# Performance work log

Hardware: AMD Instinct MI355X
Metric: run time of the kernel (lower is better)

Reference implementation:

```python
import jax, jax.numpy as jnp
import numpy as np

N_SIGMA = 1
K_MAX = 8          # max number of non-zero instance ids
FG_W = 1.0         # foreground_weight
W_INST, W_VAR, W_SEED = 1.0, 10.0, 1.0


def _lovasz_hinge_flat(logits, labels_f):
    # logits, labels_f: [P] flat; standard Lovasz hinge (descending-error sort)
    signs = 2.0 * labels_f - 1.0
    errors = 1.0 - logits * signs
    perm = jnp.argsort(-errors)
    errors_sorted = errors[perm]
    gt_sorted = labels_f[perm]
    gts = gt_sorted.sum()
    cum = jnp.cumsum(gt_sorted)
    intersection = gts - cum
    union = gts + jnp.cumsum(1.0 - gt_sorted)
    jaccard = 1.0 - intersection / union
    grad = jnp.concatenate([jaccard[:1], jaccard[1:] - jaccard[:-1]])
    return jnp.sum(jax.nn.relu(errors_sorted) * jax.lax.stop_gradient(grad))


def _spatial_emb_loss(prediction, instances, labels):
    B, C, H, W = prediction.shape
    inst = instances[:, 0]  # [B,H,W]
    # coordinate buffer: linspace over the full 1024x2048 grid, then sliced
    xm = jnp.linspace(0.0, 2.0, 2048)[:W]
    ym = jnp.linspace(0.0, 1.0, 1024)[:H]
    xym = jnp.stack([jnp.broadcast_to(xm[None, :], (H, W)),
                     jnp.broadcast_to(ym[:, None], (H, W))])  # [2,H,W]
    ids = jnp.arange(1, K_MAX + 1)

    def per_image(pred, ins, lab):
        spatial_emb = jnp.tanh(pred[0:2]) + xym            # [2,H,W]
        sigma = pred[2]                                     # [H,W] (n_sigma=1)
        seed = jax.nn.sigmoid(pred[3])                      # [H,W]
        bg = (lab == 0)
        seed_loss_bg = jnp.sum(jnp.where(bg, seed ** 2, 0.0))
        masks = (ins[None] == ids[:, None, None])           # [K,H,W]
        mf = masks.astype(pred.dtype)
        counts = mf.sum((1, 2))                             # [K]
        present = counts > 0
        cnt = jnp.maximum(counts, 1.0)
        # to_center=True: center = mean of xym over instance pixels
        center = jnp.einsum('chw,khw->kc', xym, mf) / cnt[:, None]   # [K,2]
        s_mean = jnp.einsum('hw,khw->k', sigma, mf) / cnt            # [K]
        var_k = jnp.einsum('khw,khw->k',
                           (sigma[None] - jax.lax.stop_gradient(s_mean)[:, None, None]) ** 2,
                           mf) / cnt
        s_exp = jnp.exp(10.0 * s_mean)                                # [K]
        d2 = jnp.sum((spatial_emb[None] - center[:, :, None, None]) ** 2, axis=1)  # [K,H,W]
        dist = jnp.exp(-s_exp[:, None, None] * d2)                    # [K,H,W]
        lov = jax.vmap(_lovasz_hinge_flat)(2.0 * dist.reshape(K_MAX, -1) - 1.0,
                                           mf.reshape(K_MAX, -1))     # [K]
        seed_fg = jnp.einsum('khw,khw->k',
                             (seed[None] - jax.lax.stop_gradient(dist)) ** 2, mf)
        objf = jnp.maximum(present.sum().astype(pred.dtype), 1.0)
        inst_loss = jnp.where(present, lov, 0.0).sum() / objf
        var_loss = jnp.where(present, var_k, 0.0).sum() / objf
        seed_loss = (seed_loss_bg + FG_W * jnp.where(present, seed_fg, 0.0).sum()) / (H * W)
        return W_INST * inst_loss + W_VAR * var_loss + W_SEED * seed_loss

    per = jax.vmap(per_image)(prediction, inst, labels)
    return per.mean() + 0.0 * prediction.sum()


def setup_inputs() -> dict:
    key = jax.random.key(0)
    k1, k2, k3 = jax.random.split(key, 3)
    B, H, W = 4, 512, 1024
    prediction = jax.random.normal(k1, (B, 2 + N_SIGMA + 1, H, W), dtype=jnp.float32)
    instances = jax.random.randint(k2, (B, 1, H, W), 0, K_MAX + 1, dtype=jnp.int32)
    labels = jax.random.randint(k3, (B, H, W), 0, 2, dtype=jnp.int32)
    return {"prediction": prediction, "instances": instances, "labels": labels}


def reference(prediction, instances, labels):
    return _spatial_emb_loss(prediction, instances, labels)
```

## Files before the change

kernel.cpp:

```cpp
#include <hip/hip_runtime.h>
#include <math.h>

namespace {
constexpr int B_ = 4, K_ = 8, W_ = 1024;
constexpr int N_ = 512 * 1024;
constexpr int M_ = 128;
constexpr int MP_ = M_ + 1;
constexpr int BK_ = B_ * K_;
constexpr int KM_ = K_ * M_;

constexpr int HB_ = 512;
constexpr int HBPB_ = HB_ / B_;
constexpr int HCH_ = N_ / HBPB_;
constexpr int SB_ = 1024;
constexpr int SBPB_ = SB_ / B_;
constexpr int SCH_ = N_ / SBPB_;
constexpr int NSTAT = 41;
constexpr int NHC_ = 4;

constexpr size_t PART_BYTES = (size_t)HB_ * KM_ * 4;
constexpr size_t SFG_OFF_B  = PART_BYTES;
constexpr size_t PSTAT_OFF_B = SFG_OFF_B + (size_t)BK_ * HBPB_ * 4;
constexpr size_t WSF_OFF_B  = PSTAT_OFF_B + (size_t)B_ * NSTAT * SBPB_ * 4;

constexpr int CNT_OFF  = 0;
constexpr int OBJF_OFF = 32;
}

__device__ __forceinline__ float fsigmoid_(float x) { return 1.0f / (1.0f + __expf(-x)); }
__device__ __forceinline__ float ftanh_(float x) { return 1.0f - 2.0f / (__expf(2.0f * x) + 1.0f); }

__global__ __launch_bounds__(256) void stats_kernel(const float* __restrict__ pred,
                                                    const int* __restrict__ inst,
                                                    const int* __restrict__ lab,
                                                    float* __restrict__ pstat,
                                                    float* __restrict__ out) {
    int tid = threadIdx.x;
    if (blockIdx.x == 0 && tid == 0) out[0] = 0.0f;
    int b = blockIdx.x >> 8;
    int blk = blockIdx.x & (SBPB_ - 1);
    int pix0 = blk * SCH_;

    const float* sigp = pred + ((long long)b * 4 + 2) * N_;
    const float* p3p  = pred + ((long long)b * 4 + 3) * N_;
    const int*   insp = inst + (long long)b * N_;
    const int*   labp = lab  + (long long)b * N_;

    float acc[NSTAT];
#pragma unroll
    for (int i = 0; i < NSTAT; i++) acc[i] = 0.0f;

#pragma unroll
    for (int it = 0; it < SCH_ / (256 * 4); it++) {
        int base = pix0 + (it * 256 + tid) * 4;
        float4 sg = *(const float4*)(sigp + base);
        float4 q3 = *(const float4*)(p3p + base);
        int4 in4 = *(const int4*)(insp + base);
        int4 lb4 = *(const int4*)(labp + base);
        float ss[4] = {sg.x, sg.y, sg.z, sg.w};
        float qq[4] = {q3.x, q3.y, q3.z, q3.w};
        int ii[4] = {in4.x, in4.y, in4.z, in4.w};
        int ll[4] = {lb4.x, lb4.y, lb4.z, lb4.w};
#pragma unroll
        for (int j = 0; j < 4; j++) {
            int pix = base + j;
            float xm = (float)(pix & (W_ - 1)) * (2.0f / 2047.0f);
            float ym = (float)(pix >> 10) * (1.0f / 1023.0f);
            float seed = fsigmoid_(qq[j]);
            if (ll[j] == 0) acc[40] += seed * seed;
            float s = ss[j];
#pragma unroll
            for (int k = 0; k < K_; k++) {
                float m = (ii[j] == k + 1) ? 1.0f : 0.0f;
                acc[k * 5]     += m;
                acc[k * 5 + 1] += m * xm;
                acc[k * 5 + 2] += m * ym;
                acc[k * 5 + 3] += m * s;
                acc[k * 5 + 4] += m * s * s;
            }
        }
    }
#pragma unroll
    for (int i = 0; i < NSTAT; i++) {
        float v = acc[i];
#pragma unroll
        for (int off = 32; off; off >>= 1) v += __shfl_down(v, off, 64);
        acc[i] = v;
    }
    __shared__ float xw[4][NSTAT];
    if ((tid & 63) == 0) {
        int w = tid >> 6;
#pragma unroll
        for (int i = 0; i < NSTAT; i++) xw[w][i] = acc[i];
    }
    __syncthreads();
    if (tid < NSTAT)
        pstat[((b * NSTAT + tid) << 8) + blk] =
            xw[0][tid] + xw[1][tid] + xw[2][tid] + xw[3][tid];
}

__global__ __launch_bounds__(256) void hist_kernel(const float* __restrict__ pred,
                                                   const int* __restrict__ inst,
                                                   const float* __restrict__ pstat,
                                                   float* __restrict__ wsf,
                                                   unsigned int* __restrict__ partial,
                                                   float* __restrict__ sfgpart,
                                                   float* __restrict__ out) {
    __shared__ float sq[NSTAT][4];
    __shared__ float ssum[NSTAT];
    __shared__ float prm[K_][4];
    __shared__ float svar[K_];
    __shared__ int spres[K_];
    __shared__ unsigned int hsh[NHC_][K_ * MP_];
    __shared__ float xfg[4][K_];

    int tid = threadIdx.x;
    int b = blockIdx.x >> 7;
    int blk = blockIdx.x & (HBPB_ - 1);
    int pix0 = blk * HCH_;

    if (tid < NSTAT * 4) {
        int row = tid >> 2, q = tid & 3;
        const float4* p = (const float4*)(pstat + ((size_t)(b * NSTAT + row) << 8)) + q * 16;
        float4 a = {0, 0, 0, 0};
#pragma unroll
        for (int j = 0; j < 16; j++) {
            float4 v = p[j];
            a.x += v.x; a.y += v.y; a.z += v.z; a.w += v.w;
        }
        sq[row][q] = (a.x + a.y) + (a.z + a.w);
    }
    for (int i = tid; i < NHC_ * K_ * MP_; i += 256) (&hsh[0][0])[i] = 0u;
    __syncthreads();
    if (tid < NSTAT) ssum[tid] = (sq[tid][0] + sq[tid][1]) + (sq[tid][2] + sq[tid][3]);
    __syncthreads();
    if (tid < K_) {
        float counts = ssum[tid * 5];
        float cnt = fmaxf(counts, 1.0f);
        float smean = ssum[tid * 5 + 3] / cnt;
        prm[tid][0] = ssum[tid * 5 + 1] / cnt;
        prm[tid][1] = ssum[tid * 5 + 2] / cnt;
        prm[tid][2] = expf(10.0f * smean);
        prm[tid][3] = counts;
        if (blk == 0) {
            svar[tid] = (counts > 0.0f) ? ssum[tid * 5 + 4] / cnt - smean * smean : 0.0f;
            spres[tid] = counts > 0.0f ? 1 : 0;
            wsf[CNT_OFF + b * K_ + tid] = counts;
        }
    }
    __syncthreads();
    if (blk == 0 && tid == 0) {
        float np = 0.0f, vl = 0.0f;
#pragma unroll
        for (int k = 0; k < K_; k++) { np += (float)spres[k]; vl += svar[k]; }
        float objf = fmaxf(np, 1.0f);
        wsf[OBJF_OFF + b] = objf;
        atomicAdd(out, (10.0f * vl / objf + ssum[40] / (float)N_) * (1.0f / (float)B_));
    }

    float cx[K_], cy[K_], sxp[K_];
    bool prs[K_];
#pragma unroll
    for (int k = 0; k < K_; k++) {
        cx[k] = prm[k][0]; cy[k] = prm[k][1]; sxp[k] = prm[k][2];
        prs[k] = prm[k][3] > 0.0f;
    }
    unsigned int* hpriv = &hsh[tid & 3][0];

    const float* p0p = pred + ((long long)b * 4) * N_;
    const float* p1p = p0p + N_;
    const float* p3p = p0p + 3LL * N_;
    const int* insp = inst + (long long)b * N_;

    float sfg[K_];
#pragma unroll
    for (int k = 0; k < K_; k++) sfg[k] = 0.0f;

#pragma unroll
    for (int it = 0; it < HCH_ / (256 * 4); it++) {
        int base = pix0 + (it * 256 + tid) * 4;
        float4 a0 = *(const float4*)(p0p + base);
        float4 a1 = *(const float4*)(p1p + base);
        float4 a3 = *(const float4*)(p3p + base);
        int4 in4 = *(const int4*)(insp + base);
        float v0[4] = {a0.x, a0.y, a0.z, a0.w};
        float v1[4] = {a1.x, a1.y, a1.z, a1.w};
        float v3[4] = {a3.x, a3.y, a3.z, a3.w};
        int ii[4] = {in4.x, in4.y, in4.z, in4.w};
#pragma unroll
        for (int j = 0; j < 4; j++) {
            int pix = base + j;
            float sex = ftanh_(v0[j]) + (float)(pix & (W_ - 1)) * (2.0f / 2047.0f);
            float sey = ftanh_(v1[j]) + (float)(pix >> 10) * (1.0f / 1023.0f);
            float seed = fsigmoid_(v3[j]);
            int ins = ii[j];
#pragma unroll
            for (int k = 0; k < K_; k++) {
                if (prs[k]) {
                    float dx = sex - cx[k];
                    float dy = sey - cy[k];
                    float dist = __expf(-sxp[k] * (dx * dx + dy * dy));
                    bool fg = (ins == k + 1);
                    int ib = (int)fminf(128.0f * dist, 127.0f);
                    int bin = fg ? 127 - ib : ib;
                    atomicAdd(hpriv + (k * MP_ + bin), fg ? 0x10001u : 1u);
                    if (fg) { float d = seed - dist; sfg[k] += d * d; }
                }
            }
        }
    }
    __syncthreads();

    unsigned int* gp = partial + (size_t)blockIdx.x * KM_;
    for (int i = tid; i < KM_; i += 256) {
        int r = (i >> 7) * MP_ + (i & (M_ - 1));
        gp[i] = hsh[0][r] + hsh[1][r] + hsh[2][r] + hsh[3][r];
    }

#pragma unroll
    for (int k = 0; k < K_; k++) {
        float v = sfg[k];
#pragma unroll
        for (int off = 32; off; off >>= 1) v += __shfl_down(v, off, 64);
        sfg[k] = v;
    }
    if ((tid & 63) == 0) {
        int w = tid >> 6;
#pragma unroll
        for (int k = 0; k < K_; k++) xfg[w][k] = sfg[k];
    }
    __syncthreads();
    if (tid < K_)
        sfgpart[(size_t)(b * K_ + tid) * HBPB_ + blk] =
            xfg[0][tid] + xfg[1][tid] + xfg[2][tid] + xfg[3][tid];
}

__global__ __launch_bounds__(1024) void lovasz_kernel(const unsigned int* __restrict__ partial,
                                                      const float* __restrict__ sfgpart,
                                                      const float* __restrict__ wsf,
                                                      float* __restrict__ out) {
    int bk = blockIdx.x;
    int b = bk >> 3, k = bk & 7;
    int tid = threadIdx.x;
    int bin = tid & (M_ - 1), grp = tid >> 7;
    constexpr int PER = HBPB_ / 8;

    const unsigned int* p = partial +
        (size_t)(b * HBPB_ + grp * PER) * KM_ + k * M_ + bin;
    unsigned int n = 0, f = 0;
#pragma unroll
    for (int j = 0; j < PER; j++) {
        unsigned int v = p[(size_t)j * KM_];
        n += v & 0xffffu;
        f += v >> 16;
    }

    __shared__ unsigned int gn[8][M_], gf[8][M_];
    __shared__ float lovp;
    __shared__ float xs[2];
    gn[grp][bin] = n; gf[grp][bin] = f;
    __syncthreads();

    float pcnt = wsf[CNT_OFF + bk];
    float pp = fmaxf(pcnt, 1.0f);

    if (tid < 64) {
        unsigned long long p0 = 0ull, p1 = 0ull;
#pragma unroll
        for (int g = 0; g < 8; g++) {
            uint2 vn = *(const uint2*)&gn[g][2 * tid];
            uint2 vf = *(const uint2*)&gf[g][2 * tid];
            p0 += ((unsigned long long)vn.x << 32) | (unsigned long long)vf.x;
            p1 += ((unsigned long long)vn.y << 32) | (unsigned long long)vf.y;
        }
        unsigned long long T = p0 + p1;
#pragma unroll
        for (int off = 1; off < 64; off <<= 1) {
            unsigned long long t = __shfl_down(T, off, 64);
            if (tid + off < 64) T += t;
        }
        unsigned long long S0 = T;
        unsigned long long S1 = T - p0;
        float acc;
        {
            unsigned int R = (unsigned int)(S0 >> 32), F = (unsigned int)S0;
            float J = (R == 0) ? 0.0f : (1.0f - (pp - (float)F) / (pp + (float)(R - F)));
            acc = (tid == 0 ? 0.5f : 1.0f) * J;
        }
        {
            unsigned int R = (unsigned int)(S1 >> 32), F = (unsigned int)S1;
            float J = (R == 0) ? 0.0f : (1.0f - (pp - (float)F) / (pp + (float)(R - F)));
            acc += J;
        }
#pragma unroll
        for (int off = 32; off; off >>= 1) acc += __shfl_down(acc, off, 64);
        if (tid == 0) lovp = acc;
    } else if (tid >= 256 && tid < 384) {
        float sv = sfgpart[(size_t)bk * HBPB_ + (tid - 256)];
#pragma unroll
        for (int off = 32; off; off >>= 1) sv += __shfl_down(sv, off, 64);
        if ((tid & 63) == 0) xs[(tid - 256) >> 6] = sv;
    }
    __syncthreads();

    if (tid == 0 && pcnt > 0.0f) {
        float lov = lovp * (2.0f / (float)M_);
        float sfgt = xs[0] + xs[1];
        float objf = wsf[OBJF_OFF + b];
        atomicAdd(out, (lov / objf + sfgt / (float)N_) * (1.0f / (float)B_));
    }
}

extern "C" void kernel_launch(void* const* d_in, const int* in_sizes, int n_in,
                              void* d_out, int out_size, void* d_ws, size_t ws_size,
                              hipStream_t stream) {
    const float* pred = (const float*)d_in[0];
    const int* inst = (const int*)d_in[1];
    const int* lab = (const int*)d_in[2];
    float* out = (float*)d_out;

    unsigned int* partial = (unsigned int*)d_ws;
    float* sfgpart = (float*)((char*)d_ws + SFG_OFF_B);
    float* pstat = (float*)((char*)d_ws + PSTAT_OFF_B);
    float* wsf = (float*)((char*)d_ws + WSF_OFF_B);

    stats_kernel<<<SB_, 256, 0, stream>>>(pred, inst, lab, pstat, out);
    hist_kernel<<<HB_, 256, 0, stream>>>(pred, inst, pstat, wsf, partial, sfgpart, out);
    lovasz_kernel<<<BK_, 1024, 0, stream>>>(partial, sfgpart, wsf, out);
}
```

Measured before the change: 116.5 us.

## Fuse Lovasz finalization into hist kernel via last-blocks ticket counter

Removes the separate lovasz_kernel launch. Each hist block takes a per-image atomic ticket, and the last four blocks of each image spin-wait until all blocks of that image have finished. Each of those blocks then reduces the partial histograms and sfg sums for two instance ids and computes the Lovasz term. This saves one launch and its gap, but the final reduction now runs in only 16 blocks of 256 threads instead of 32 blocks of 1024 threads. It also relies on spin-waiting, which needs all blocks of an image to be resident or to finish without deadlock.

```diff
diff --git a/kernel.cpp b/kernel.cpp
--- a/kernel.cpp
+++ b/kernel.cpp
@@ -17,14 +17,12 @@
 constexpr int SCH_ = N_ / SBPB_;
 constexpr int NSTAT = 41;
 constexpr int NHC_ = 4;
+constexpr int NFIN_ = 4;
 
 constexpr size_t PART_BYTES = (size_t)HB_ * KM_ * 4;
 constexpr size_t SFG_OFF_B  = PART_BYTES;
 constexpr size_t PSTAT_OFF_B = SFG_OFF_B + (size_t)BK_ * HBPB_ * 4;
-constexpr size_t WSF_OFF_B  = PSTAT_OFF_B + (size_t)B_ * NSTAT * SBPB_ * 4;
-
-constexpr int CNT_OFF  = 0;
-constexpr int OBJF_OFF = 32;
+constexpr size_t CTR_OFF_B  = PSTAT_OFF_B + (size_t)B_ * NSTAT * SBPB_ * 4;
 }
 
 __device__ __forceinline__ float fsigmoid_(float x) { return 1.0f / (1.0f + __expf(-x)); }
@@ -34,9 +32,13 @@
                                                     const int* __restrict__ inst,
                                                     const int* __restrict__ lab,
                                                     float* __restrict__ pstat,
+                                                    unsigned int* __restrict__ ctr,
                                                     float* __restrict__ out) {
     int tid = threadIdx.x;
-    if (blockIdx.x == 0 && tid == 0) out[0] = 0.0f;
+    if (blockIdx.x == 0) {
+        if (tid == 0) out[0] = 0.0f;
+        if (tid < B_) ctr[tid] = 0u;
+    }
     int b = blockIdx.x >> 8;
     int blk = blockIdx.x & (SBPB_ - 1);
     int pix0 = blk * SCH_;
@@ -102,9 +104,9 @@
 __global__ __launch_bounds__(256) void hist_kernel(const float* __restrict__ pred,
                                                    const int* __restrict__ inst,
                                                    const float* __restrict__ pstat,
-                                                   float* __restrict__ wsf,
                                                    unsigned int* __restrict__ partial,
                                                    float* __restrict__ sfgpart,
+                                                   unsigned int* __restrict__ ctr,
                                                    float* __restrict__ out) {
     __shared__ float sq[NSTAT][4];
     __shared__ float ssum[NSTAT];
@@ -113,6 +115,9 @@
     __shared__ int spres[K_];
     __shared__ unsigned int hsh[NHC_][K_ * MP_];
     __shared__ float xfg[4][K_];
+    __shared__ unsigned int stkt;
+    __shared__ unsigned int fgn[2][M_], fgf[2][M_];
+    __shared__ float flov, fxs[2];
 
     int tid = threadIdx.x;
     int b = blockIdx.x >> 7;
@@ -145,7 +150,6 @@
         if (blk == 0) {
             svar[tid] = (counts > 0.0f) ? ssum[tid * 5 + 4] / cnt - smean * smean : 0.0f;
             spres[tid] = counts > 0.0f ? 1 : 0;
-            wsf[CNT_OFF + b * K_ + tid] = counts;
         }
     }
     __syncthreads();
@@ -154,7 +158,6 @@
 #pragma unroll
         for (int k = 0; k < K_; k++) { np += (float)spres[k]; vl += svar[k]; }
         float objf = fmaxf(np, 1.0f);
-        wsf[OBJF_OFF + b] = objf;
         atomicAdd(out, (10.0f * vl / objf + ssum[40] / (float)N_) * (1.0f / (float)B_));
     }
 
@@ -233,81 +236,90 @@
     if (tid < K_)
         sfgpart[(size_t)(b * K_ + tid) * HBPB_ + blk] =
             xfg[0][tid] + xfg[1][tid] + xfg[2][tid] + xfg[3][tid];
-}
-
-__global__ __launch_bounds__(1024) void lovasz_kernel(const unsigned int* __restrict__ partial,
-                                                      const float* __restrict__ sfgpart,
-                                                      const float* __restrict__ wsf,
-                                                      float* __restrict__ out) {
-    int bk = blockIdx.x;
-    int b = bk >> 3, k = bk & 7;
-    int tid = threadIdx.x;
-    int bin = tid & (M_ - 1), grp = tid >> 7;
-    constexpr int PER = HBPB_ / 8;
-
-    const unsigned int* p = partial +
-        (size_t)(b * HBPB_ + grp * PER) * KM_ + k * M_ + bin;
-    unsigned int n = 0, f = 0;
-#pragma unroll
-    for (int j = 0; j < PER; j++) {
-        unsigned int v = p[(size_t)j * KM_];
-        n += v & 0xffffu;
-        f += v >> 16;
-    }
-
-    __shared__ unsigned int gn[8][M_], gf[8][M_];
-    __shared__ float lovp;
-    __shared__ float xs[2];
-    gn[grp][bin] = n; gf[grp][bin] = f;
-    __syncthreads();
-
-    float pcnt = wsf[CNT_OFF + bk];
-    float pp = fmaxf(pcnt, 1.0f);
-
-    if (tid < 64) {
-        unsigned long long p0 = 0ull, p1 = 0ull;
-#pragma unroll
-        for (int g = 0; g < 8; g++) {
-            uint2 vn = *(const uint2*)&gn[g][2 * tid];
-            uint2 vf = *(const uint2*)&gf[g][2 * tid];
-            p0 += ((unsigned long long)vn.x << 32) | (unsigned long long)vf.x;
-            p1 += ((unsigned long long)vn.y << 32) | (unsigned long long)vf.y;
-        }
-        unsigned long long T = p0 + p1;
-#pragma unroll
-        for (int off = 1; off < 64; off <<= 1) {
-            unsigned long long t = __shfl_down(T, off, 64);
-            if (tid + off < 64) T += t;
-        }
-        unsigned long long S0 = T;
-        unsigned long long S1 = T - p0;
-        float acc;
-        {
-            unsigned int R = (unsigned int)(S0 >> 32), F = (unsigned int)S0;
-            float J = (R == 0) ? 0.0f : (1.0f - (pp - (float)F) / (pp + (float)(R - F)));
-            acc = (tid == 0 ? 0.5f : 1.0f) * J;
-        }
-        {
-            unsigned int R = (unsigned int)(S1 >> 32), F = (unsigned int)S1;
-            float J = (R == 0) ? 0.0f : (1.0f - (pp - (float)F) / (pp + (float)(R - F)));
-            acc += J;
-        }
-#pragma unroll
-        for (int off = 32; off; off >>= 1) acc += __shfl_down(acc, off, 64);
-        if (tid == 0) lovp = acc;
-    } else if (tid >= 256 && tid < 384) {
-        float sv = sfgpart[(size_t)bk * HBPB_ + (tid - 256)];
-#pragma unroll
-        for (int off = 32; off; off >>= 1) sv += __shfl_down(sv, off, 64);
-        if ((tid & 63) == 0) xs[(tid - 256) >> 6] = sv;
-    }
-    __syncthreads();
-
-    if (tid == 0 && pcnt > 0.0f) {
-        float lov = lovp * (2.0f / (float)M_);
-        float sfgt = xs[0] + xs[1];
-        float objf = wsf[OBJF_OFF + b];
-        atomicAdd(out, (lov / objf + sfgt / (float)N_) * (1.0f / (float)B_));
+
+    __threadfence();
+    __syncthreads();
+    if (tid == 0) stkt = atomicAdd(&ctr[b], 1u);
+    __syncthreads();
+    unsigned int tkt = stkt;
+    if (tkt < (unsigned int)(HBPB_ - NFIN_)) return;
+
+    if (tid == 0) {
+        while (__hip_atomic_load(&ctr[b], __ATOMIC_ACQUIRE, __HIP_MEMORY_SCOPE_AGENT)
+               < (unsigned int)HBPB_)
+            __builtin_amdgcn_s_sleep(2);
+    }
+    __syncthreads();
+
+    int which = (int)tkt - (HBPB_ - NFIN_);
+    int binn = tid & (M_ - 1), h = tid >> 7;
+
+    for (int kk = 0; kk < 2; kk++) {
+        int k = 2 * which + kk;
+        float pcnt = prm[k][3];
+        float pp = fmaxf(pcnt, 1.0f);
+
+        const unsigned int* prt = partial +
+            (size_t)(b * HBPB_ + h * (HBPB_ / 2)) * KM_ + k * M_ + binn;
+        unsigned int n = 0, f = 0;
+#pragma unroll 8
+        for (int j = 0; j < HBPB_ / 2; j++) {
+            unsigned int v = prt[(size_t)j * KM_];
+            n += v & 0xffffu;
+            f += v >> 16;
+        }
+        fgn[h][binn] = n; fgf[h][binn] = f;
+        __syncthreads();
+
+        if (tid < 64) {
+            uint2 vn0 = *(const uint2*)&fgn[0][2 * tid];
+            uint2 vf0 = *(const uint2*)&fgf[0][2 * tid];
+            uint2 vn1 = *(const uint2*)&fgn[1][2 * tid];
+            uint2 vf1 = *(const uint2*)&fgf[1][2 * tid];
+            unsigned long long p0 =
+                ((unsigned long long)(vn0.x + vn1.x) << 32) | (unsigned long long)(vf0.x + vf1.x);
+            unsigned long long p1 =
+                ((unsigned long long)(vn0.y + vn1.y) << 32) | (unsigned long long)(vf0.y + vf1.y);
+            unsigned long long T = p0 + p1;
+#pragma unroll
+            for (int off = 1; off < 64; off <<= 1) {
+                unsigned long long t = __shfl_down(T, off, 64);
+                if (tid + off < 64) T += t;
+            }
+            unsigned long long S0 = T;
+            unsigned long long S1 = T - p0;
+            float acc;
+            {
+                unsigned int R = (unsigned int)(S0 >> 32), F = (unsigned int)S0;
+                float J = (R == 0) ? 0.0f : (1.0f - (pp - (float)F) / (pp + (float)(R - F)));
+                acc = (tid == 0 ? 0.5f : 1.0f) * J;
+            }
+            {
+                unsigned int R = (unsigned int)(S1 >> 32), F = (unsigned int)S1;
+                float J = (R == 0) ? 0.0f : (1.0f - (pp - (float)F) / (pp + (float)(R - F)));
+                acc += J;
+            }
+#pragma unroll
+            for (int off = 32; off; off >>= 1) acc += __shfl_down(acc, off, 64);
+            if (tid == 0) flov = acc;
+        } else if (tid >= 128 && tid < 256) {
+            float sv = sfgpart[(size_t)(b * K_ + k) * HBPB_ + (tid - 128)];
+#pragma unroll
+            for (int off = 32; off; off >>= 1) sv += __shfl_down(sv, off, 64);
+            if ((tid & 63) == 0) fxs[(tid - 128) >> 6] = sv;
+        }
+        __syncthreads();
+
+        if (tid == 0 && pcnt > 0.0f) {
+            float np = 0.0f;
+#pragma unroll
+            for (int j = 0; j < K_; j++) np += (prm[j][3] > 0.0f) ? 1.0f : 0.0f;
+            float objf = fmaxf(np, 1.0f);
+            float lov = flov * (2.0f / (float)M_);
+            float sfgt = fxs[0] + fxs[1];
+            atomicAdd(out, (lov / objf + sfgt / (float)N_) * (1.0f / (float)B_));
+        }
+        __syncthreads();
     }
 }
 
@@ -322,9 +334,8 @@
     unsigned int* partial = (unsigned int*)d_ws;
     float* sfgpart = (float*)((char*)d_ws + SFG_OFF_B);
     float* pstat = (float*)((char*)d_ws + PSTAT_OFF_B);
-    float* wsf = (float*)((char*)d_ws + WSF_OFF_B);
-
-    stats_kernel<<<SB_, 256, 0, stream>>>(pred, inst, lab, pstat, out);
-    hist_kernel<<<HB_, 256, 0, stream>>>(pred, inst, pstat, wsf, partial, sfgpart, out);
-    lovasz_kernel<<<BK_, 1024, 0, stream>>>(partial, sfgpart, wsf, out);
+    unsigned int* ctr = (unsigned int*)((char*)d_ws + CTR_OFF_B);
+
+    stats_kernel<<<SB_, 256, 0, stream>>>(pred, inst, lab, pstat, ctr, out);
+    hist_kernel<<<HB_, 256, 0, stream>>>(pred, inst, pstat, partial, sfgpart, ctr, out);
 }
```

Result: slower. 159.8 us (+37.2%).

## Merge per-block histograms with global atomics instead of a partial buffer

Applied to the files above, without the earlier changes.

Each hist block now adds its summed 8x128 histogram directly into per-image global count arrays (total and foreground kept separately) with atomicAdd, skipping zero entries. This replaces writing a 512x1024-entry partial buffer that the lovasz kernel had to read and reduce. The stats kernel zeroes the global histograms, and the lovasz kernel shrinks to 256 threads that just load 128 bins. In exchange there is atomic contention on the global histogram, since 128 blocks write into each image's bins.

```diff
diff --git a/kernel.cpp b/kernel.cpp
--- a/kernel.cpp
+++ b/kernel.cpp
@@ -18,10 +18,11 @@
 constexpr int NSTAT = 41;
 constexpr int NHC_ = 4;
 
-constexpr size_t PART_BYTES = (size_t)HB_ * KM_ * 4;
-constexpr size_t SFG_OFF_B  = PART_BYTES;
-constexpr size_t PSTAT_OFF_B = SFG_OFF_B + (size_t)BK_ * HBPB_ * 4;
-constexpr size_t WSF_OFF_B  = PSTAT_OFF_B + (size_t)B_ * NSTAT * SBPB_ * 4;
+constexpr size_t GHN_OFF_W  = 0;
+constexpr size_t GHF_OFF_W  = GHN_OFF_W + B_ * KM_;
+constexpr size_t SFG_OFF_W  = GHF_OFF_W + B_ * KM_;
+constexpr size_t PSTAT_OFF_W = SFG_OFF_W + (size_t)BK_ * HBPB_;
+constexpr size_t WSF_OFF_W  = PSTAT_OFF_W + (size_t)B_ * NSTAT * SBPB_;
 
 constexpr int CNT_OFF  = 0;
 constexpr int OBJF_OFF = 32;
@@ -34,9 +35,13 @@
                                                     const int* __restrict__ inst,
                                                     const int* __restrict__ lab,
                                                     float* __restrict__ pstat,
+                                                    unsigned int* __restrict__ gh,
                                                     float* __restrict__ out) {
     int tid = threadIdx.x;
-    if (blockIdx.x == 0 && tid == 0) out[0] = 0.0f;
+    if (blockIdx.x < 32) {
+        gh[blockIdx.x * 256 + tid] = 0u;
+        if (blockIdx.x == 0 && tid == 0) out[0] = 0.0f;
+    }
     int b = blockIdx.x >> 8;
     int blk = blockIdx.x & (SBPB_ - 1);
     int pix0 = blk * SCH_;
@@ -103,7 +108,8 @@
                                                    const int* __restrict__ inst,
                                                    const float* __restrict__ pstat,
                                                    float* __restrict__ wsf,
-                                                   unsigned int* __restrict__ partial,
+                                                   unsigned int* __restrict__ ghn,
+                                                   unsigned int* __restrict__ ghf,
                                                    float* __restrict__ sfgpart,
                                                    float* __restrict__ out) {
     __shared__ float sq[NSTAT][4];
@@ -211,10 +217,14 @@
     }
     __syncthreads();
 
-    unsigned int* gp = partial + (size_t)blockIdx.x * KM_;
     for (int i = tid; i < KM_; i += 256) {
         int r = (i >> 7) * MP_ + (i & (M_ - 1));
-        gp[i] = hsh[0][r] + hsh[1][r] + hsh[2][r] + hsh[3][r];
+        unsigned int s = hsh[0][r] + hsh[1][r] + hsh[2][r] + hsh[3][r];
+        if (s) {
+            atomicAdd(&ghn[b * KM_ + i], s & 0xffffu);
+            unsigned int hi = s >> 16;
+            if (hi) atomicAdd(&ghf[b * KM_ + i], hi);
+        }
     }
 
 #pragma unroll
@@ -235,44 +245,32 @@
             xfg[0][tid] + xfg[1][tid] + xfg[2][tid] + xfg[3][tid];
 }
 
-__global__ __launch_bounds__(1024) void lovasz_kernel(const unsigned int* __restrict__ partial,
-                                                      const float* __restrict__ sfgpart,
-                                                      const float* __restrict__ wsf,
-                                                      float* __restrict__ out) {
+__global__ __launch_bounds__(256) void lovasz_kernel(const unsigned int* __restrict__ ghn,
+                                                     const unsigned int* __restrict__ ghf,
+                                                     const float* __restrict__ sfgpart,
+                                                     const float* __restrict__ wsf,
+                                                     float* __restrict__ out) {
     int bk = blockIdx.x;
     int b = bk >> 3, k = bk & 7;
     int tid = threadIdx.x;
-    int bin = tid & (M_ - 1), grp = tid >> 7;
-    constexpr int PER = HBPB_ / 8;
-
-    const unsigned int* p = partial +
-        (size_t)(b * HBPB_ + grp * PER) * KM_ + k * M_ + bin;
-    unsigned int n = 0, f = 0;
-#pragma unroll
-    for (int j = 0; j < PER; j++) {
-        unsigned int v = p[(size_t)j * KM_];
-        n += v & 0xffffu;
-        f += v >> 16;
-    }
-
-    __shared__ unsigned int gn[8][M_], gf[8][M_];
+
+    __shared__ unsigned int sn[M_], sf[M_];
     __shared__ float lovp;
     __shared__ float xs[2];
-    gn[grp][bin] = n; gf[grp][bin] = f;
+    if (tid < M_) {
+        sn[tid] = ghn[(size_t)b * KM_ + k * M_ + tid];
+        sf[tid] = ghf[(size_t)b * KM_ + k * M_ + tid];
+    }
     __syncthreads();
 
     float pcnt = wsf[CNT_OFF + bk];
     float pp = fmaxf(pcnt, 1.0f);
 
     if (tid < 64) {
-        unsigned long long p0 = 0ull, p1 = 0ull;
-#pragma unroll
-        for (int g = 0; g < 8; g++) {
-            uint2 vn = *(const uint2*)&gn[g][2 * tid];
-            uint2 vf = *(const uint2*)&gf[g][2 * tid];
-            p0 += ((unsigned long long)vn.x << 32) | (unsigned long long)vf.x;
-            p1 += ((unsigned long long)vn.y << 32) | (unsigned long long)vf.y;
-        }
+        uint2 vn = *(const uint2*)&sn[2 * tid];
+        uint2 vf = *(const uint2*)&sf[2 * tid];
+        unsigned long long p0 = ((unsigned long long)vn.x << 32) | (unsigned long long)vf.x;
+        unsigned long long p1 = ((unsigned long long)vn.y << 32) | (unsigned long long)vf.y;
         unsigned long long T = p0 + p1;
 #pragma unroll
         for (int off = 1; off < 64; off <<= 1) {
@@ -295,11 +293,11 @@
 #pragma unroll
         for (int off = 32; off; off >>= 1) acc += __shfl_down(acc, off, 64);
         if (tid == 0) lovp = acc;
-    } else if (tid >= 256 && tid < 384) {
-        float sv = sfgpart[(size_t)bk * HBPB_ + (tid - 256)];
+    } else if (tid >= 128) {
+        float sv = sfgpart[(size_t)bk * HBPB_ + (tid - 128)];
 #pragma unroll
         for (int off = 32; off; off >>= 1) sv += __shfl_down(sv, off, 64);
-        if ((tid & 63) == 0) xs[(tid - 256) >> 6] = sv;
+        if ((tid & 63) == 0) xs[(tid - 128) >> 6] = sv;
     }
     __syncthreads();
 
@@ -319,12 +317,14 @@
     const int* lab = (const int*)d_in[2];
     float* out = (float*)d_out;
 
-    unsigned int* partial = (unsigned int*)d_ws;
-    float* sfgpart = (float*)((char*)d_ws + SFG_OFF_B);
-    float* pstat = (float*)((char*)d_ws + PSTAT_OFF_B);
-    float* wsf = (float*)((char*)d_ws + WSF_OFF_B);
-
-    stats_kernel<<<SB_, 256, 0, stream>>>(pred, inst, lab, pstat, out);
-    hist_kernel<<<HB_, 256, 0, stream>>>(pred, inst, pstat, wsf, partial, sfgpart, out);
-    lovasz_kernel<<<BK_, 1024, 0, stream>>>(partial, sfgpart, wsf, out);
-}
+    unsigned int* gh = (unsigned int*)d_ws;
+    unsigned int* ghn = gh + GHN_OFF_W;
+    unsigned int* ghf = gh + GHF_OFF_W;
+    float* sfgpart = (float*)d_ws + SFG_OFF_W;
+    float* pstat = (float*)d_ws + PSTAT_OFF_W;
+    float* wsf = (float*)d_ws + WSF_OFF_W;
+
+    stats_kernel<<<SB_, 256, 0, stream>>>(pred, inst, lab, pstat, gh, out);
+    hist_kernel<<<HB_, 256, 0, stream>>>(pred, inst, pstat, wsf, ghn, ghf, sfgpart, out);
+    lovasz_kernel<<<BK_, 256, 0, stream>>>(ghn, ghf, sfgpart, wsf, out);
+}
```

Measured after the change: 117.4 us. About the same (+0.8%).
